# Kernel tuning notes

Hardware: AMD Instinct MI355X
Metric: run time of the kernel (lower is better)

Reference implementation:

```python
import jax, jax.numpy as jnp
import numpy as np

HEADS = 16


def setup_inputs() -> dict:
    key = jax.random.key(0)
    ks = jax.random.split(key, 7)
    B, N, MEM, DIM = 2, 2048, 2048, 1024
    J = MEM + N
    x = jax.random.normal(ks[0], (B, N, DIM), dtype=jnp.float32)
    mem = jax.random.normal(ks[1], (B, MEM, DIM), dtype=jnp.float32)
    expire_mask = jax.random.uniform(ks[2], (B, 1, 1, J), dtype=jnp.float32)
    Wq = jax.random.normal(ks[3], (DIM, DIM), dtype=jnp.float32) * 0.02
    Wkv = jax.random.normal(ks[4], (DIM, 2 * DIM), dtype=jnp.float32) * 0.02
    Wo = jax.random.normal(ks[5], (DIM, DIM), dtype=jnp.float32) * 0.02
    bo = jnp.zeros((DIM,), dtype=jnp.float32)
    return {"x": x, "mem": mem, "expire_mask": expire_mask,
            "Wq": Wq, "Wkv": Wkv, "Wo": Wo, "bo": bo}


def reference(x, mem, expire_mask, Wq, Wkv, Wo, bo):
    b, n, dim = x.shape
    h = HEADS
    d = dim // h
    scale = d ** -0.5
    mem_len = mem.shape[1]

    q = x @ Wq                                   # [b, n, dim]
    context = jnp.concatenate([mem, x], axis=1)  # [b, j, dim]
    kv = context @ Wkv                           # [b, j, 2*dim]
    k, v = jnp.split(kv, 2, axis=-1)

    def to_heads(t):
        bb, nn, _ = t.shape
        return t.reshape(bb, nn, h, d).transpose(0, 2, 1, 3)  # b h n d

    q, k, v = map(to_heads, (q, k, v))

    dots = jnp.einsum('bhid,bhjd->bhij', q, k) * scale  # [b,h,n,j]
    j_len = dots.shape[-1]
    # causal mask with memory offset: position i attends to j <= i + mem_len
    i_idx = jnp.arange(n)[:, None]
    j_idx = jnp.arange(j_len)[None, :]
    causal = j_idx > (i_idx + mem_len)           # True => masked
    dots = jnp.where(causal[None, None], -jnp.inf, dots)

    attn = jax.nn.softmax(dots, axis=-1)
    attn = attn * expire_mask                    # post-softmax expire gating

    out = jnp.einsum('bhij,bhjd->bhid', attn, v)  # [b,h,n,d]
    out = out.transpose(0, 2, 1, 3).reshape(b, n, dim)
    return out @ Wo + bo
```

## Files before the change

kernel.cpp:

```cpp
#include <hip/hip_runtime.h>
#include <cstdint>

typedef __bf16 bf16_t;
typedef __attribute__((ext_vector_type(2))) __bf16 bf16x2;
typedef __attribute__((ext_vector_type(4))) __bf16 bf16x4;
typedef __attribute__((ext_vector_type(8))) __bf16 bf16x8;
typedef __attribute__((ext_vector_type(4))) float f32x4;
typedef __attribute__((ext_vector_type(16))) float f32x16;
typedef __attribute__((ext_vector_type(4))) int i32x4;

constexpr int Bx = 2, Nx = 2048, MEMx = 2048, Jx = 4096, DIMx = 1024, Hx = 16, HDx = 64;

__device__ __forceinline__ void gload_lds16(const bf16_t* g, bf16_t* lds) {
  __builtin_amdgcn_global_load_lds(
      (const __attribute__((address_space(1))) unsigned int*)g,
      (__attribute__((address_space(3))) unsigned int*)lds, 16, 0, 0);
}

__device__ __forceinline__ int pk2(float a, float b) {
  bf16x2 t;
  t[0] = (bf16_t)a;
  t[1] = (bf16_t)b;
  return __builtin_bit_cast(int, t);
}

__device__ __forceinline__ void pl32swap(int& a, int& b) {
  asm volatile("v_permlane32_swap_b32 %0, %1" : "+v"(a), "+v"(b));
}

__device__ __forceinline__ float fmax3(float a, float b, float c) {
  float d;
  asm("v_max3_f32 %0, %1, %2, %3" : "=v"(d) : "v"(a), "v"(b), "v"(c));
  return d;
}

__global__ void k_build_bf16(const float* __restrict__ x, const float* __restrict__ mem,
                             bf16_t* __restrict__ xb, bf16_t* __restrict__ ctxb) {
  const int XT = Bx * Nx * DIMx;
  const int CT = Bx * Jx * DIMx;
  for (int i = blockIdx.x * blockDim.x + threadIdx.x; i < XT + CT;
       i += gridDim.x * blockDim.x) {
    if (i < XT) {
      xb[i] = (bf16_t)x[i];
    } else {
      int c = i - XT;
      int bb = c / (Jx * DIMx);
      int rr = c % (Jx * DIMx);
      int j = rr / DIMx, d = rr % DIMx;
      float v = (j < MEMx) ? mem[(int64_t)(bb * MEMx + j) * DIMx + d]
                           : x[(int64_t)(bb * Nx + (j - MEMx)) * DIMx + d];
      ctxb[c] = (bf16_t)v;
    }
  }
}

__global__ void k_transpose_w(const float* __restrict__ W, bf16_t* __restrict__ WT,
                              int K, int Nc) {
  int total = K * Nc;
  for (int i = blockIdx.x * blockDim.x + threadIdx.x; i < total;
       i += gridDim.x * blockDim.x) {
    int n = i / K, k = i % K;
    WT[i] = (bf16_t)W[(int64_t)k * Nc + n];
  }
}

template <int MODE>
__launch_bounds__(256)
__global__ void k_gemm_bt(const bf16_t* __restrict__ A, const bf16_t* __restrict__ BT,
                          void* __restrict__ Cv, const float* __restrict__ bias,
                          const float* __restrict__ gate, bf16_t* __restrict__ VT,
                          float scale, int M, int Nc, int K) {
  __shared__ bf16_t As[2][128 * 32];
  __shared__ bf16_t Bs[2][128 * 32];
  const int tid = threadIdx.x;
  const int w = tid >> 6, l = tid & 63;
  const int lr = l & 15, lg = l >> 4;
  const int m0 = blockIdx.y * 128, n0 = blockIdx.x * 128;
  const int wm = (w >> 1) * 64, wn = (w & 1) * 64;

  const int srow = w * 16 + (l >> 2);
  const int scol = (l & 3) * 8;
  const bf16_t* ga0 = A + (int64_t)(m0 + srow) * K + scol;
  const bf16_t* gb0 = BT + (int64_t)(n0 + srow) * K + scol;

  auto stage = [&](int bufi, int k0) {
    bf16_t* lA = &As[bufi][0] + w * 512;
    bf16_t* lB = &Bs[bufi][0] + w * 512;
    gload_lds16(ga0 + k0, lA);
    gload_lds16(ga0 + (int64_t)64 * K + k0, lA + 2048);
    gload_lds16(gb0 + k0, lB);
    gload_lds16(gb0 + (int64_t)64 * K + k0, lB + 2048);
  };

  f32x4 acc[4][4] = {};

  const int nsteps = K >> 5;
  stage(0, 0);
  stage(1, 32);

  for (int t = 0; t < nsteps; ++t) {
    const int cur = t & 1;
    if (t + 1 < nsteps)
      asm volatile("s_waitcnt vmcnt(4)" ::: "memory");
    else
      asm volatile("s_waitcnt vmcnt(0)" ::: "memory");
    __builtin_amdgcn_s_barrier();
    __builtin_amdgcn_sched_barrier(0);

    bf16x8 af[4], bfr[4];
#pragma unroll
    for (int q = 0; q < 4; ++q)
      af[q] = *(const bf16x8*)(&As[cur][0] + (wm + q * 16 + lr) * 32 + lg * 8);
#pragma unroll
    for (int q = 0; q < 4; ++q)
      bfr[q] = *(const bf16x8*)(&Bs[cur][0] + (wn + q * 16 + lr) * 32 + lg * 8);
#pragma unroll
    for (int mt = 0; mt < 4; ++mt)
#pragma unroll
      for (int nt = 0; nt < 4; ++nt)
        acc[mt][nt] = __builtin_amdgcn_mfma_f32_16x16x32_bf16(af[mt], bfr[nt],
                                                              acc[mt][nt], 0, 0, 0);
    __builtin_amdgcn_s_barrier();
    __builtin_amdgcn_sched_barrier(0);
    if (t + 2 < nsteps) stage(cur, (t + 2) << 5);
  }

#pragma unroll
  for (int mt = 0; mt < 4; ++mt) {
#pragma unroll
    for (int nt = 0; nt < 4; ++nt) {
      int col = n0 + wn + nt * 16 + lr;
      int row0 = m0 + wm + mt * 16 + lg * 4;
      if constexpr (MODE == 0) {
#pragma unroll
        for (int r = 0; r < 4; ++r)
          ((bf16_t*)Cv)[(int64_t)(row0 + r) * Nc + col] =
              (bf16_t)(acc[mt][nt][r] * scale);
      } else if constexpr (MODE == 1) {
#pragma unroll
        for (int r = 0; r < 4; ++r)
          ((float*)Cv)[(int64_t)(row0 + r) * Nc + col] = acc[mt][nt][r] + bias[col];
      } else {
        if (col < 1024) {
#pragma unroll
          for (int r = 0; r < 4; ++r)
            ((bf16_t*)Cv)[(int64_t)(row0 + r) * 1024 + col] = (bf16_t)acc[mt][nt][r];
        } else {
          int hh = (col - 1024) >> 6, dd = col & 63;
          int bb = row0 >> 12, jj = row0 & (Jx - 1);
          bf16x4 ov;
#pragma unroll
          for (int r = 0; r < 4; ++r)
            ov[r] = (bf16_t)(acc[mt][nt][r] * gate[row0 + r]);
          *(bf16x4*)(VT + (((int64_t)(bb * Hx + hh) * HDx + dd) << 12) + jj) = ov;
        }
      }
    }
  }
}

__launch_bounds__(256)
__global__ void k_attn(const bf16_t* __restrict__ Q, const bf16_t* __restrict__ Kbuf,
                       const bf16_t* __restrict__ VT, bf16_t* __restrict__ Opart,
                       float2* __restrict__ ML) {
  __shared__ bf16_t Ks[2][64 * 64];
  __shared__ bf16_t Vs[2][64 * 64];

  const int tid = threadIdx.x;
  const int w = tid >> 6, l = tid & 63;
  const int ql = l & 31, hi = l >> 5;

  const int lin = blockIdx.x;
  const int qi0 = lin & 15, h = (lin >> 4) & 15;
  const int c = (lin >> 8) & 1, b = lin >> 9;
  const int qi = b ? (15 - qi0) : qi0;
  const int q0 = qi * 128;

  const bf16_t* Qb = Q + ((int64_t)b * Nx) * DIMx + h * HDx;
  const bf16_t* Kb = Kbuf + ((int64_t)b * Jx) * 1024 + h * HDx;
  const bf16_t* Vb = VT + ((int64_t)(b * Hx + h) * HDx << 12);

  const int qrow = q0 + w * 32 + ql;

  bf16x8 qf[4];
#pragma unroll
  for (int dt = 0; dt < 4; ++dt)
    qf[dt] = *(const bf16x8*)(Qb + (int64_t)qrow * DIMx + dt * 16 + hi * 8);
  asm volatile("s_waitcnt vmcnt(0)" ::: "memory");

  int koff[2][4], voff[2][4];
#pragma unroll
  for (int jb = 0; jb < 2; ++jb)
#pragma unroll
    for (int dt = 0; dt < 4; ++dt)
      koff[jb][dt] = (jb * 32 + ql) * 128 + (((dt * 2 + hi) * 16) ^ ((ql & 7) * 16));
#pragma unroll
  for (int db = 0; db < 2; ++db)
#pragma unroll
    for (int jt = 0; jt < 4; ++jt)
      voff[db][jt] = (db * 32 + ql) * 128 + (((jt * 2 + hi) * 16) ^ ((ql & 7) * 16));

  bf16x8 onesv;
#pragma unroll
  for (int i = 0; i < 8; ++i) onesv[i] = (bf16_t)1.0f;

  f32x16 o[2] = {};
  f32x16 ol = {};
  float mrun = 8.0f;

  const int srow8 = l >> 3;
  const int swcol = ((l & 7) ^ srow8) * 8;
  const int jstart = c * 2048;
  const int jend = c ? ((Jx < q0 + 128 + MEMx) ? Jx : (q0 + 128 + MEMx)) : 2048;
  const int nt_tiles = (jend - jstart) >> 6;
  const f32x16 z16 = {};

  const bf16_t* ksrc0 = Kb + (int64_t)(w * 16 + srow8) * 1024 + swcol;
  const bf16_t* vsrc0 = Vb + (int64_t)(w * 16 + srow8) * Jx + swcol;

  auto stage = [&](int bufi, int j0) {
    bf16_t* kd = &Ks[bufi][0] + w * 1024;
    const bf16_t* ks = ksrc0 + (int64_t)j0 * 1024;
    gload_lds16(ks, kd);
    gload_lds16(ks + 8 * 1024, kd + 512);
    bf16_t* vd = &Vs[bufi][0] + w * 1024;
    const bf16_t* vs = vsrc0 + j0;
    gload_lds16(vs, vd);
    gload_lds16(vs + 8 * Jx, vd + 512);
  };

  stage(0, jstart);
  stage(1, jstart + 64);

  for (int t = 0; t < nt_tiles; ++t) {
    const int cur = t & 1;
    const int j0 = jstart + (t << 6);
    if (t + 1 < nt_tiles)
      asm volatile("s_waitcnt vmcnt(4)" ::: "memory");
    else
      asm volatile("s_waitcnt vmcnt(0)" ::: "memory");
    __builtin_amdgcn_s_barrier();
    __builtin_amdgcn_sched_barrier(0);

    const char* KsC = (const char*)&Ks[cur][0];
    const char* VsC = (const char*)&Vs[cur][0];

    f32x16 s[2];
    __builtin_amdgcn_s_setprio(1);
#pragma unroll
    for (int jb = 0; jb < 2; ++jb) {
      f32x16 acc = z16;
#pragma unroll
      for (int dt = 0; dt < 4; ++dt) {
        bf16x8 kf = *(const bf16x8*)(KsC + koff[jb][dt]);
        acc = __builtin_amdgcn_mfma_f32_32x32x16_bf16(kf, qf[dt], acc, 0, 0, 0);
      }
      s[jb] = acc;
    }
    __builtin_amdgcn_s_setprio(0);

    if (j0 + 63 > q0 + MEMx) {
#pragma unroll
      for (int jb = 0; jb < 2; ++jb)
#pragma unroll
        for (int r = 0; r < 16; ++r) {
          int j = j0 + jb * 32 + (r & 3) + (r >> 2) * 8 + hi * 4;
          if (j > qrow + MEMx) s[jb][r] = -1e30f;
        }
    }

    float t12[12];
#pragma unroll
    for (int i = 0; i < 10; ++i)
      t12[i] = fmax3(s[(3 * i) >> 4][(3 * i) & 15], s[(3 * i + 1) >> 4][(3 * i + 1) & 15],
                     s[(3 * i + 2) >> 4][(3 * i + 2) & 15]);
    t12[10] = s[1][14];
    t12[11] = s[1][15];
    float t4[4];
#pragma unroll
    for (int i = 0; i < 4; ++i) t4[i] = fmax3(t12[3 * i], t12[3 * i + 1], t12[3 * i + 2]);
    float tm = fmaxf(fmax3(t4[0], t4[1], t4[2]), t4[3]);
    tm = fmaxf(tm, __shfl_xor(tm, 32));

    if (!__all(tm <= mrun + 8.f)) {
      float mnew = fmaxf(mrun, tm);
      float al = exp2f(mrun - mnew);
      mrun = mnew;
#pragma unroll
      for (int r = 0; r < 16; ++r) ol[r] *= al;
#pragma unroll
      for (int db = 0; db < 2; ++db)
#pragma unroll
        for (int r = 0; r < 16; ++r) o[db][r] *= al;
    }

#pragma unroll
    for (int jb = 0; jb < 2; ++jb)
#pragma unroll
      for (int r = 0; r < 16; ++r) s[jb][r] = exp2f(s[jb][r] - mrun);

    bf16x8 pfrag[4];
#pragma unroll
    for (int jb = 0; jb < 2; ++jb) {
      int pw[8];
#pragma unroll
      for (int g = 0; g < 8; ++g) pw[g] = pk2(s[jb][2 * g], s[jb][2 * g + 1]);
      pl32swap(pw[0], pw[2]);
      pl32swap(pw[1], pw[3]);
      pl32swap(pw[4], pw[6]);
      pl32swap(pw[5], pw[7]);
      i32x4 f0 = {pw[0], pw[1], pw[2], pw[3]};
      i32x4 f1 = {pw[4], pw[5], pw[6], pw[7]};
      pfrag[jb * 2] = __builtin_bit_cast(bf16x8, f0);
      pfrag[jb * 2 + 1] = __builtin_bit_cast(bf16x8, f1);
    }

    __builtin_amdgcn_s_setprio(1);
#pragma unroll
    for (int jt = 0; jt < 4; ++jt) {
      bf16x8 vf0 = *(const bf16x8*)(VsC + voff[0][jt]);
      o[0] = __builtin_amdgcn_mfma_f32_32x32x16_bf16(vf0, pfrag[jt], o[0], 0, 0, 0);
      bf16x8 vf1 = *(const bf16x8*)(VsC + voff[1][jt]);
      o[1] = __builtin_amdgcn_mfma_f32_32x32x16_bf16(vf1, pfrag[jt], o[1], 0, 0, 0);
      ol = __builtin_amdgcn_mfma_f32_32x32x16_bf16(onesv, pfrag[jt], ol, 0, 0, 0);
    }
    __builtin_amdgcn_s_setprio(0);

    __builtin_amdgcn_s_barrier();
    __builtin_amdgcn_sched_barrier(0);
    if (t + 2 < nt_tiles) stage(cur, jstart + ((t + 2) << 6));
  }

  bf16_t* op = Opart + (int64_t)c * (Bx * Nx * DIMx) +
               (int64_t)(b * Nx + qrow) * DIMx + h * HDx;
#pragma unroll
  for (int db = 0; db < 2; ++db)
#pragma unroll
    for (int g = 0; g < 4; ++g) {
      bf16x4 ov;
#pragma unroll
      for (int r = 0; r < 4; ++r) ov[r] = (bf16_t)o[db][g * 4 + r];
      *(bf16x4*)(op + db * 32 + g * 8 + hi * 4) = ov;
    }
  if (hi == 0)
    ML[((int64_t)(c * Bx + b) * Hx + h) * Nx + qrow] = make_float2(mrun, ol[0]);
}

__global__ void k_combine(const bf16_t* __restrict__ Op, const float2* __restrict__ ML,
                          bf16_t* __restrict__ Ho) {
  const int64_t CH = (int64_t)Bx * Nx * DIMx;
  int i = blockIdx.x * blockDim.x + threadIdx.x;
  const int total = (int)(CH >> 3);
  if (i >= total) return;
  int64_t off = (int64_t)i * 8;
  int bqh = (int)(off >> 6);
  int h = bqh & 15;
  int bq = bqh >> 4;
  int b = bq >> 11, q = bq & (Nx - 1);
  float2 ml0 = ML[((int64_t)b * Hx + h) * Nx + q];
  float2 ml1 = ML[((int64_t)(Bx + b) * Hx + h) * Nx + q];
  float M = fmaxf(ml0.x, ml1.x);
  float a0 = exp2f(ml0.x - M), a1 = exp2f(ml1.x - M);
  float inv = 1.f / (a0 * ml0.y + a1 * ml1.y);
  a0 *= inv;
  a1 *= inv;
  bf16x8 v0 = *(const bf16x8*)(Op + off);
  bf16x8 v1 = *(const bf16x8*)(Op + CH + off);
  bf16x8 outv;
#pragma unroll
  for (int r = 0; r < 8; ++r)
    outv[r] = (bf16_t)(a0 * (float)v0[r] + a1 * (float)v1[r]);
  *(bf16x8*)(Ho + off) = outv;
}

extern "C" void kernel_launch(void* const* d_in, const int* in_sizes, int n_in,
                              void* d_out, int out_size, void* d_ws, size_t ws_size,
                              hipStream_t stream) {
  const float* x    = (const float*)d_in[0];
  const float* mem  = (const float*)d_in[1];
  const float* expm = (const float*)d_in[2];
  const float* Wq   = (const float*)d_in[3];
  const float* Wkv  = (const float*)d_in[4];
  const float* Wo   = (const float*)d_in[5];
  const float* bo   = (const float*)d_in[6];
  float* out = (float*)d_out;

  bf16_t* p = (bf16_t*)d_ws;
  bf16_t* xb   = p; p += (size_t)Bx * Nx * DIMx;
  bf16_t* ctxb = p; p += (size_t)Bx * Jx * DIMx;
  bf16_t* WqT  = p; p += (size_t)DIMx * DIMx;
  bf16_t* WkvT = p; p += (size_t)DIMx * 2 * DIMx;
  bf16_t* WoT  = p; p += (size_t)DIMx * DIMx;
  bf16_t* Qb   = p; p += (size_t)Bx * Nx * DIMx;
  bf16_t* KVb  = p; p += (size_t)Bx * Jx * 2 * DIMx;
  bf16_t* Ho   = p; p += (size_t)Bx * Nx * DIMx;

  bf16_t* Kbuf = KVb;
  bf16_t* VT   = KVb + (size_t)Bx * Jx * 1024;
  bf16_t* Opart = ctxb;
  float2* ML    = (float2*)xb;

  k_build_bf16<<<4096, 256, 0, stream>>>(x, mem, xb, ctxb);
  k_transpose_w<<<1024, 256, 0, stream>>>(Wq, WqT, DIMx, DIMx);
  k_transpose_w<<<2048, 256, 0, stream>>>(Wkv, WkvT, DIMx, 2 * DIMx);
  k_transpose_w<<<1024, 256, 0, stream>>>(Wo, WoT, DIMx, DIMx);

  const float qscale = 0.125f * 1.4426950408889634f;
  k_gemm_bt<0><<<dim3(1024 / 128, 4096 / 128), 256, 0, stream>>>(
      xb, WqT, Qb, nullptr, nullptr, nullptr, qscale, Bx * Nx, DIMx, DIMx);
  k_gemm_bt<2><<<dim3(2048 / 128, 8192 / 128), 256, 0, stream>>>(
      ctxb, WkvT, Kbuf, nullptr, expm, VT, 1.0f, Bx * Jx, 2 * DIMx, DIMx);

  k_attn<<<1024, 256, 0, stream>>>(Qb, Kbuf, VT, Opart, ML);
  k_combine<<<(Bx * Nx * DIMx / 8 + 255) / 256, 256, 0, stream>>>(Opart, ML, Ho);

  k_gemm_bt<1><<<dim3(1024 / 128, 4096 / 128), 256, 0, stream>>>(
      Ho, WoT, out, bo, nullptr, nullptr, 1.0f, Bx * Nx, DIMx, DIMx);
}
```

Baseline: 270.7 us.

## Vectorize bf16 conversion, tile weight transposes, balance attention split-K halves

```diff
diff --git a/kernel.cpp b/kernel.cpp
--- a/kernel.cpp
+++ b/kernel.cpp
@@ -34,34 +34,47 @@
   return d;
 }
 
-__global__ void k_build_bf16(const float* __restrict__ x, const float* __restrict__ mem,
-                             bf16_t* __restrict__ xb, bf16_t* __restrict__ ctxb) {
-  const int XT = Bx * Nx * DIMx;
-  const int CT = Bx * Jx * DIMx;
-  for (int i = blockIdx.x * blockDim.x + threadIdx.x; i < XT + CT;
+__global__ void k_build8(const float* __restrict__ x, const float* __restrict__ mem,
+                         bf16_t* __restrict__ xb, bf16_t* __restrict__ ctxb) {
+  const int XT8 = (Bx * Nx * DIMx) >> 3;
+  const int CT8 = (Bx * Jx * DIMx) >> 3;
+  for (int i = blockIdx.x * blockDim.x + threadIdx.x; i < XT8 + CT8;
        i += gridDim.x * blockDim.x) {
-    if (i < XT) {
-      xb[i] = (bf16_t)x[i];
+    const float* src;
+    bf16_t* dst;
+    if (i < XT8) {
+      src = x + ((int64_t)i << 3);
+      dst = xb + ((int64_t)i << 3);
     } else {
-      int c = i - XT;
-      int bb = c / (Jx * DIMx);
-      int rr = c % (Jx * DIMx);
-      int j = rr / DIMx, d = rr % DIMx;
-      float v = (j < MEMx) ? mem[(int64_t)(bb * MEMx + j) * DIMx + d]
-                           : x[(int64_t)(bb * Nx + (j - MEMx)) * DIMx + d];
-      ctxb[c] = (bf16_t)v;
-    }
+      int64_t c = (int64_t)(i - XT8) << 3;
+      int bb = (int)(c >> 22);
+      int rr = (int)(c & ((1 << 22) - 1));
+      int j = rr >> 10, d = rr & 1023;
+      src = (j < MEMx) ? mem + (((int64_t)(bb * MEMx + j)) << 10) + d
+                       : x + (((int64_t)(bb * Nx + (j - MEMx))) << 10) + d;
+      dst = ctxb + c;
+    }
+    float4 a = *(const float4*)src;
+    float4 b = *(const float4*)(src + 4);
+    bf16x8 v;
+    v[0] = (bf16_t)a.x; v[1] = (bf16_t)a.y; v[2] = (bf16_t)a.z; v[3] = (bf16_t)a.w;
+    v[4] = (bf16_t)b.x; v[5] = (bf16_t)b.y; v[6] = (bf16_t)b.z; v[7] = (bf16_t)b.w;
+    *(bf16x8*)dst = v;
   }
 }
 
-__global__ void k_transpose_w(const float* __restrict__ W, bf16_t* __restrict__ WT,
-                              int K, int Nc) {
-  int total = K * Nc;
-  for (int i = blockIdx.x * blockDim.x + threadIdx.x; i < total;
-       i += gridDim.x * blockDim.x) {
-    int n = i / K, k = i % K;
-    WT[i] = (bf16_t)W[(int64_t)k * Nc + n];
-  }
+__global__ void k_transpose_tiled(const float* __restrict__ W, bf16_t* __restrict__ WT,
+                                  int K, int Nc) {
+  __shared__ bf16_t t[32][33];
+  const int tx = threadIdx.x & 31, ty = threadIdx.x >> 5;
+  const int n0 = blockIdx.x * 32, k0 = blockIdx.y * 32;
+#pragma unroll
+  for (int r = 0; r < 4; ++r)
+    t[ty + 8 * r][tx] = (bf16_t)W[(int64_t)(k0 + ty + 8 * r) * Nc + n0 + tx];
+  __syncthreads();
+#pragma unroll
+  for (int r = 0; r < 4; ++r)
+    WT[(int64_t)(n0 + ty + 8 * r) * K + k0 + tx] = t[tx][ty + 8 * r];
 }
 
 template <int MODE>
@@ -210,9 +223,11 @@
 
   const int srow8 = l >> 3;
   const int swcol = ((l & 7) ^ srow8) * 8;
-  const int jstart = c * 2048;
-  const int jend = c ? ((Jx < q0 + 128 + MEMx) ? Jx : (q0 + 128 + MEMx)) : 2048;
-  const int nt_tiles = (jend - jstart) >> 6;
+  const int jend_full = (Jx < q0 + 128 + MEMx) ? Jx : (q0 + 128 + MEMx);
+  const int T = jend_full >> 6;
+  const int half = T >> 1;
+  const int jstart = c ? (half << 6) : 0;
+  const int nt_tiles = c ? (T - half) : half;
   const f32x16 z16 = {};
 
   const bf16_t* ksrc0 = Kb + (int64_t)(w * 16 + srow8) * 1024 + swcol;
@@ -400,10 +415,10 @@
   bf16_t* Opart = ctxb;
   float2* ML    = (float2*)xb;
 
-  k_build_bf16<<<4096, 256, 0, stream>>>(x, mem, xb, ctxb);
-  k_transpose_w<<<1024, 256, 0, stream>>>(Wq, WqT, DIMx, DIMx);
-  k_transpose_w<<<2048, 256, 0, stream>>>(Wkv, WkvT, DIMx, 2 * DIMx);
-  k_transpose_w<<<1024, 256, 0, stream>>>(Wo, WoT, DIMx, DIMx);
+  k_build8<<<2048, 256, 0, stream>>>(x, mem, xb, ctxb);
+  k_transpose_tiled<<<dim3(32, 32), 256, 0, stream>>>(Wq, WqT, DIMx, DIMx);
+  k_transpose_tiled<<<dim3(64, 32), 256, 0, stream>>>(Wkv, WkvT, DIMx, 2 * DIMx);
+  k_transpose_tiled<<<dim3(32, 32), 256, 0, stream>>>(Wo, WoT, DIMx, DIMx);
 
   const float qscale = 0.125f * 1.4426950408889634f;
   k_gemm_bt<0><<<dim3(1024 / 128, 4096 / 128), 256, 0, stream>>>(
```

Result: faster. 254.3 us (-6.1%).
